# Optimization experiments

Measured on AMD Instinct MI355X. Metric: run time of the kernel, lower is better.

Reference implementation:

```python
import jax, jax.numpy as jnp
import numpy as np

B, G, N, P, E, F, K = 8, 256, 1024, 4, 1, 256, 4
ZERO_TOL = 1e-9
INF = 1e12
ATT_SLOPE = 0.2  # leaky relu slope inside attention


def setup_inputs() -> dict:
    key = jax.random.key(0)
    ks = jax.random.split(key, 6)
    stdv = float(1.0 / np.sqrt(G * P))
    x = jax.random.normal(ks[0], (B, G, N), jnp.float32)
    mixer = jax.random.uniform(ks[1], (P, E, 2 * F), jnp.float32, -stdv, stdv)
    weight = jax.random.uniform(ks[2], (P, E, F, G), jnp.float32, -stdv, stdv)
    weight_bias = jnp.zeros((P, E, F), jnp.float32)  # reset_parameters inits to 0
    filterWeight = jax.random.uniform(ks[3], (P, F, E, K, G), jnp.float32, -stdv, stdv)
    bias = jax.random.uniform(ks[4], (F, 1), jnp.float32, -stdv, stdv)
    adj = (jax.random.uniform(ks[5], (B, E, N, N)) < 0.05).astype(jnp.float32)
    S = jnp.maximum(adj, jnp.eye(N, dtype=jnp.float32)[None, None])
    return dict(x=x, mixer=mixer, weight=weight, weight_bias=weight_bias,
                filterWeight=filterWeight, bias=bias, S=S)


def reference(x, mixer, weight, weight_bias, filterWeight, bias, S):
    # --- learnAttentionGSOBatch ---
    # Wx: [B,P,E,F,N]
    Wx = jnp.einsum('pefg,bgn->bpefn', weight, x) + weight_bias[None, :, :, :, None]
    a1 = mixer[..., :F]   # [P,E,F]
    a2 = mixer[..., F:]   # [P,E,F]
    e1 = jnp.einsum('pef,bpefn->bpen', a1, Wx)  # a1^T W x_j
    e2 = jnp.einsum('pef,bpefn->bpen', a2, Wx)  # a2^T W x_i
    # aWx[b,p,e,i,j] = e1[j] + e2[i]  (matches a1Wx + a2Wx^T broadcast)
    aWx = e1[..., None, :] + e2[..., :, None]   # [B,P,E,N,N]
    eij = jax.nn.leaky_relu(aWx, ATT_SLOPE)
    mask = (jnp.sum(jnp.abs(S), axis=1)[:, None, None] > ZERO_TOL).astype(x.dtype)  # [B,1,1,N,N]
    aij = jax.nn.softmax(eij * mask - (1.0 - mask) * INF, axis=-1) * mask  # [B,P,E,N,N]

    # --- K-hop polynomial filter ---
    xk = jnp.broadcast_to(x[:, None, None], (B, P, E, G, N))
    zs = [xk]
    for _ in range(1, K):
        xk = jnp.matmul(xk, aij)        # diffuse along attention GSO
        zs.append(xk)
    z = jnp.stack(zs, axis=3)            # [B,P,E,K,G,N]
    # h reshape [P,F,E*K*G] contracted against z reshaped [B,P,N,E*K*G]
    y = jnp.einsum('bpekgn,pfekg->bpfn', z, filterWeight) + bias  # bias [F,1] broadcasts

    # --- forward wrapper: nonlinearity (leaky_relu, default slope 0.01) + head concat ---
    y = jax.nn.leaky_relu(y)                              # [B,P,F,N]
    y = jnp.transpose(y, (0, 3, 1, 2)).reshape(B, N, P * F)
    return jnp.transpose(y, (0, 2, 1))                    # [B, P*F, N]
```

## Files before the change

kernel.cpp:

```cpp
#include <hip/hip_runtime.h>
#include <hip/hip_bf16.h>

#define B_ 8
#define G_ 256
#define N_ 1024
#define P_ 4
#define F_ 256
#define KHOP 4
#define KG_ (KHOP * G_)

typedef unsigned short ushort_t;
typedef __bf16 bf16x8 __attribute__((ext_vector_type(8)));
typedef unsigned short u16x8 __attribute__((ext_vector_type(8)));
typedef float f32x4 __attribute__((ext_vector_type(4)));

__device__ __forceinline__ unsigned short f2bf(float f) {
  union { float fl; unsigned int i; } v; v.fl = f;
  return (unsigned short)((v.i + 0x7fffu + ((v.i >> 16) & 1u)) >> 16);
}

__device__ __forceinline__ void gload_lds16(const ushort_t* g, ushort_t* l) {
  __builtin_amdgcn_global_load_lds(
      (const __attribute__((address_space(1))) void*)g,
      (__attribute__((address_space(3))) void*)l, 16, 0, 0);
}

__global__ __launch_bounds__(256) void k_prep(
    const float* __restrict__ x, const float* __restrict__ mixer,
    const float* __restrict__ weight, const float* __restrict__ wb,
    const float* __restrict__ fw, float* __restrict__ e1, float* __restrict__ e2,
    ushort_t* __restrict__ fwbf, ushort_t* __restrict__ xT,
    float* __restrict__ sumb) {
  int blk = blockIdx.x;
  int t = threadIdx.x;
  if (blk < 128) {
    __shared__ float s1[G_], s2[G_];
    __shared__ float cred[2][4];
    int bp = blk >> 2;
    int nc = blk & 3;
    int b = bp >> 2, p = bp & (P_ - 1);
    int n = nc * 256 + t;
    float acc1 = 0.f, acc2 = 0.f;
    const float* wp = weight + (size_t)p * F_ * G_ + t;
    const float* mp = mixer + p * 2 * F_;
    for (int f = 0; f < F_; ++f) {
      float wv = wp[(size_t)f * G_];
      acc1 = fmaf(mp[f], wv, acc1);
      acc2 = fmaf(mp[F_ + f], wv, acc2);
    }
    s1[t] = acc1;
    s2[t] = acc2;
    float c1p = mp[t] * wb[p * F_ + t];
    float c2p = mp[F_ + t] * wb[p * F_ + t];
#pragma unroll
    for (int mask = 1; mask < 64; mask <<= 1) {
      c1p += __shfl_xor(c1p, mask, 64);
      c2p += __shfl_xor(c2p, mask, 64);
    }
    if ((t & 63) == 0) {
      cred[0][t >> 6] = c1p;
      cred[1][t >> 6] = c2p;
    }
    __syncthreads();
    float c1 = cred[0][0] + cred[0][1] + cred[0][2] + cred[0][3];
    float c2 = cred[1][0] + cred[1][1] + cred[1][2] + cred[1][3];
    const float* xb = x + (size_t)b * G_ * N_ + n;
    float a1 = 0.f, a2 = 0.f;
#pragma unroll 8
    for (int g = 0; g < G_; ++g) {
      float xv = xb[(size_t)g * N_];
      a1 = fmaf(s1[g], xv, a1);
      a2 = fmaf(s2[g], xv, a2);
    }
    e1[(size_t)bp * N_ + n] = c1 + a1;
    e2[(size_t)bp * N_ + n] = c2 + a2;
  } else if (blk < 128 + 1024) {
    int i = (blk - 128) * 1024 + t * 4;
    float4 v = *(const float4*)&fw[i];
    ushort4 o;
    o.x = f2bf(v.x); o.y = f2bf(v.y); o.z = f2bf(v.z); o.w = f2bf(v.w);
    *(ushort4*)&fwbf[i] = o;
  } else if (blk < 1152 + 512) {
    __shared__ ushort_t tile[64][66];
    int idx = blk - 1152;
    int n0 = (idx & 15) * 64;
    int g0 = ((idx >> 4) & 3) * 64;
    int b = idx >> 6;
    int rr = t >> 4, cc = (t & 15) * 4;
#pragma unroll
    for (int ps = 0; ps < 4; ++ps) {
      float4 v = *(const float4*)&x[((size_t)b * G_ + g0 + ps * 16 + rr) * N_ + n0 + cc];
      tile[ps * 16 + rr][cc] = f2bf(v.x);
      tile[ps * 16 + rr][cc + 1] = f2bf(v.y);
      tile[ps * 16 + rr][cc + 2] = f2bf(v.z);
      tile[ps * 16 + rr][cc + 3] = f2bf(v.w);
    }
    __syncthreads();
#pragma unroll
    for (int ps = 0; ps < 4; ++ps) {
      int nl = ps * 16 + rr;
      int gl = cc;
      ushort4 o;
      o.x = tile[gl][nl];
      o.y = tile[gl + 1][nl];
      o.z = tile[gl + 2][nl];
      o.w = tile[gl + 3][nl];
      *(ushort4*)&xT[((size_t)b * N_ + n0 + nl) * G_ + g0 + gl] = o;
    }
  } else {
    int i = (blk - 1664) * 256 + t;
    sumb[i] = 0.f;
  }
}

__global__ __launch_bounds__(256) void k_att(const float* __restrict__ e1,
                                             const float* __restrict__ e2,
                                             const float* __restrict__ S,
                                             ushort_t* __restrict__ expT,
                                             float* __restrict__ sumb) {
  __shared__ ushort_t tile[256][72];
  __shared__ float se1[256];
  __shared__ float se2[64];
  int bp = blockIdx.z;
  int b = bp >> 2;
  int i0 = blockIdx.y * 64;
  int jt = blockIdx.x;
  int j0 = jt * 256;
  int t = threadIdx.x;
  int rr = t >> 4;
  int cc4 = t & 15;
  int cc = cc4 * 4;

  se1[t] = e1[(size_t)bp * N_ + j0 + t];
  if (t < 64) se2[t] = e2[(size_t)bp * N_ + i0 + t];
  __syncthreads();

  const float* Sb = S + (size_t)b * N_ * N_;
  float re2[4];
#pragma unroll
  for (int ps = 0; ps < 4; ++ps) re2[ps] = se2[ps * 16 + rr];
  float psum[4] = {0.f, 0.f, 0.f, 0.f};
#pragma unroll
  for (int js = 0; js < 4; ++js) {
    float4 e1q = *(float4*)&se1[js * 64 + cc];
    float e1v[4] = {e1q.x, e1q.y, e1q.z, e1q.w};
#pragma unroll
    for (int ps = 0; ps < 4; ++ps) {
      int il = ps * 16 + rr;
      float4 s4 = *(const float4*)&Sb[(size_t)(i0 + il) * N_ + j0 + js * 64 + cc];
      float sv[4] = {s4.x, s4.y, s4.z, s4.w};
#pragma unroll
      for (int s = 0; s < 4; ++s) {
        float v = e1v[s] + re2[ps];
        float l = v >= 0.f ? v : 0.2f * v;
        bool m = fabsf(sv[s]) > 1e-9f;
        float e = m ? __expf(l) : 0.f;
        psum[ps] += e;
        tile[js * 64 + cc + s][il] = f2bf(e);
      }
    }
  }
#pragma unroll
  for (int mask = 1; mask < 16; mask <<= 1) {
#pragma unroll
    for (int ps = 0; ps < 4; ++ps) psum[ps] += __shfl_xor(psum[ps], mask, 64);
  }
  if (cc4 == 0) {
#pragma unroll
    for (int ps = 0; ps < 4; ++ps)
      atomicAdd(&sumb[(size_t)bp * N_ + i0 + ps * 16 + rr], psum[ps]);
  }
  __syncthreads();
  ushort_t* Tb = expT + (size_t)bp * N_ * N_;
  int jl0 = t >> 3;
  int ig = (t & 7) * 8;
#pragma unroll
  for (int pass = 0; pass < 8; ++pass) {
    int jl = pass * 32 + jl0;
    u16x8 v = *(const u16x8*)&tile[jl][ig];
    *(u16x8*)&Tb[(size_t)(j0 + jl) * N_ + i0 + ig] = v;
  }
}

__global__ __launch_bounds__(256, 2) void gemm_step(
    const ushort_t* __restrict__ Aprev, const ushort_t* __restrict__ Bt,
    const ushort_t* __restrict__ fwbf, const ushort_t* __restrict__ xT,
    const float* __restrict__ bias, const float* __restrict__ sumb,
    ushort_t* __restrict__ outb, float* __restrict__ outf,
    int kslice, int has_prev, int last) {
  __shared__ ushort_t As[2][128 * 32];
  __shared__ ushort_t Bs[2][128 * 32];
  int bp = blockIdx.z;
  int p = bp & (P_ - 1), b = bp >> 2;
  int n0 = blockIdx.x * 128, m0 = blockIdx.y * 128;
  int t = threadIdx.x;
  int lane = t & 63;
  int w = t >> 6;
  int wm = w >> 1, wn = w & 1;
  int lr = lane & 15, quad = lane >> 4;
  int rowL = t >> 2;
  int colL = (t & 3) * 8;
  int ldsoff = (t & ~63) * 8;

  const ushort_t* A1 = Aprev + (size_t)bp * (F_ * N_) + (size_t)(m0 + rowL) * N_ + colL;
  const ushort_t* B1 = Bt + (size_t)bp * N_ * N_ + (size_t)(n0 + rowL) * N_ + colL;
  const ushort_t* A2 = fwbf + (size_t)p * (F_ * KG_) + (size_t)(m0 + rowL) * KG_ +
                       kslice * G_ + colL;
  const ushort_t* B2 = xT + (size_t)b * (N_ * G_) + (size_t)(n0 + rowL) * G_ + colL;

  f32x4 acc[4][4] = {};

  if (has_prev) {
    for (int kt = 0; kt < N_; kt += 64) {
      __syncthreads();
      gload_lds16(A1 + kt, &As[0][ldsoff]);
      gload_lds16(A1 + (size_t)64 * N_ + kt, &As[0][2048 + ldsoff]);
      gload_lds16(A1 + kt + 32, &As[1][ldsoff]);
      gload_lds16(A1 + (size_t)64 * N_ + kt + 32, &As[1][2048 + ldsoff]);
      gload_lds16(B1 + kt, &Bs[0][ldsoff]);
      gload_lds16(B1 + (size_t)64 * N_ + kt, &Bs[0][2048 + ldsoff]);
      gload_lds16(B1 + kt + 32, &Bs[1][ldsoff]);
      gload_lds16(B1 + (size_t)64 * N_ + kt + 32, &Bs[1][2048 + ldsoff]);
      __syncthreads();
#pragma unroll
      for (int c = 0; c < 2; ++c) {
        bf16x8 af[4], bfr[4];
#pragma unroll
        for (int mi = 0; mi < 4; ++mi)
          af[mi] = __builtin_bit_cast(bf16x8,
              *(const u16x8*)&As[c][(wm * 64 + mi * 16 + lr) * 32 + quad * 8]);
#pragma unroll
        for (int ni = 0; ni < 4; ++ni)
          bfr[ni] = __builtin_bit_cast(bf16x8,
              *(const u16x8*)&Bs[c][(wn * 64 + ni * 16 + lr) * 32 + quad * 8]);
#pragma unroll
        for (int mi = 0; mi < 4; ++mi)
#pragma unroll
          for (int ni = 0; ni < 4; ++ni)
            acc[mi][ni] = __builtin_amdgcn_mfma_f32_16x16x32_bf16(af[mi], bfr[ni], acc[mi][ni], 0, 0, 0);
      }
    }
  }
  for (int gt = 0; gt < G_; gt += 64) {
    __syncthreads();
    gload_lds16(A2 + gt, &As[0][ldsoff]);
    gload_lds16(A2 + (size_t)64 * KG_ + gt, &As[0][2048 + ldsoff]);
    gload_lds16(A2 + gt + 32, &As[1][ldsoff]);
    gload_lds16(A2 + (size_t)64 * KG_ + gt + 32, &As[1][2048 + ldsoff]);
    gload_lds16(B2 + gt, &Bs[0][ldsoff]);
    gload_lds16(B2 + (size_t)64 * G_ + gt, &Bs[0][2048 + ldsoff]);
    gload_lds16(B2 + gt + 32, &Bs[1][ldsoff]);
    gload_lds16(B2 + (size_t)64 * G_ + gt + 32, &Bs[1][2048 + ldsoff]);
    __syncthreads();
#pragma unroll
    for (int c = 0; c < 2; ++c) {
      bf16x8 af[4], bfr[4];
#pragma unroll
      for (int mi = 0; mi < 4; ++mi)
        af[mi] = __builtin_bit_cast(bf16x8,
            *(const u16x8*)&As[c][(wm * 64 + mi * 16 + lr) * 32 + quad * 8]);
#pragma unroll
      for (int ni = 0; ni < 4; ++ni)
        bfr[ni] = __builtin_bit_cast(bf16x8,
            *(const u16x8*)&Bs[c][(wn * 64 + ni * 16 + lr) * 32 + quad * 8]);
#pragma unroll
      for (int mi = 0; mi < 4; ++mi)
#pragma unroll
        for (int ni = 0; ni < 4; ++ni)
          acc[mi][ni] = __builtin_amdgcn_mfma_f32_16x16x32_bf16(af[mi], bfr[ni], acc[mi][ni], 0, 0, 0);
    }
  }

  if (last) {
    float* Ob = outf + (size_t)bp * (F_ * N_);
#pragma unroll
    for (int mi = 0; mi < 4; ++mi) {
      int fbase = m0 + wm * 64 + mi * 16 + quad * 4;
#pragma unroll
      for (int ni = 0; ni < 4; ++ni) {
        int n = n0 + wn * 64 + ni * 16 + lr;
#pragma unroll
        for (int r = 0; r < 4; ++r) {
          float v = acc[mi][ni][r] + bias[fbase + r];
          Ob[(size_t)(fbase + r) * N_ + n] = v >= 0.f ? v : 0.01f * v;
        }
      }
    }
  } else {
    ushort_t* Ob = outb + (size_t)bp * (F_ * N_);
    float iv[4];
#pragma unroll
    for (int ni = 0; ni < 4; ++ni)
      iv[ni] = 1.0f / sumb[(size_t)bp * N_ + n0 + wn * 64 + ni * 16 + lr];
#pragma unroll
    for (int mi = 0; mi < 4; ++mi) {
      int fbase = m0 + wm * 64 + mi * 16 + quad * 4;
#pragma unroll
      for (int ni = 0; ni < 4; ++ni) {
        int n = n0 + wn * 64 + ni * 16 + lr;
#pragma unroll
        for (int r = 0; r < 4; ++r)
          Ob[(size_t)(fbase + r) * N_ + n] = f2bf(acc[mi][ni][r] * iv[ni]);
      }
    }
  }
}

extern "C" void kernel_launch(void* const* d_in, const int* in_sizes, int n_in,
                              void* d_out, int out_size, void* d_ws, size_t ws_size,
                              hipStream_t stream) {
  const float* x = (const float*)d_in[0];
  const float* mixer = (const float*)d_in[1];
  const float* weight = (const float*)d_in[2];
  const float* wb = (const float*)d_in[3];
  const float* fw = (const float*)d_in[4];
  const float* bias = (const float*)d_in[5];
  const float* S = (const float*)d_in[6];
  float* out = (float*)d_out;

  char* ws = (char*)d_ws;
  size_t off = 0;
  auto take = [&](size_t bytes) -> char* {
    char* p = ws + off;
    off = (off + bytes + 255) & ~(size_t)255;
    return p;
  };
  float* e1 = (float*)take((size_t)B_ * P_ * N_ * 4);
  float* e2 = (float*)take((size_t)B_ * P_ * N_ * 4);
  float* sumb = (float*)take((size_t)B_ * P_ * N_ * 4);
  ushort_t* fwbf = (ushort_t*)take((size_t)P_ * F_ * KHOP * G_ * 2);
  ushort_t* xT = (ushort_t*)take((size_t)B_ * N_ * G_ * 2);
  ushort_t* expT = (ushort_t*)take((size_t)B_ * P_ * N_ * N_ * 2);
  ushort_t* sA = (ushort_t*)take((size_t)B_ * P_ * F_ * N_ * 2);
  ushort_t* sB = (ushort_t*)take((size_t)B_ * P_ * F_ * N_ * 2);

  k_prep<<<1792, 256, 0, stream>>>(x, mixer, weight, wb, fw, e1, e2, fwbf, xT, sumb);
  k_att<<<dim3(4, 16, 32), 256, 0, stream>>>(e1, e2, S, expT, sumb);

  dim3 gg(8, 2, 32);
  gemm_step<<<gg, 256, 0, stream>>>(nullptr, expT, fwbf, xT, bias, sumb, sA, nullptr, 3, 0, 0);
  gemm_step<<<gg, 256, 0, stream>>>(sA, expT, fwbf, xT, bias, sumb, sB, nullptr, 2, 1, 0);
  gemm_step<<<gg, 256, 0, stream>>>(sB, expT, fwbf, xT, bias, sumb, sA, nullptr, 1, 1, 0);
  gemm_step<<<gg, 256, 0, stream>>>(sA, expT, fwbf, xT, bias, sumb, nullptr, out, 0, 1, 1);
}
```

Measured before the change: 258.0 us.

## Double-buffer GEMM LDS tiles and remap blocks so each XCD owns whole batches

The two K-loops of the Horner-style GEMM step are merged into one loop. Global-to-LDS loads now use a double-buffered pipeline: the next tile is issued before computing the current one, with explicit vmcnt waits and barriers. Launch is flattened to a 1D grid that maps blocks so each XCD handles four (b,p) slices, keeping each expT matrix's reuse within one L2. This doubles LDS use to 64KB per block, which may reduce occupancy under launch_bounds(256,2).

```diff
diff --git a/kernel.cpp b/kernel.cpp
--- a/kernel.cpp
+++ b/kernel.cpp
@@ -188,11 +188,16 @@
     const float* __restrict__ bias, const float* __restrict__ sumb,
     ushort_t* __restrict__ outb, float* __restrict__ outf,
     int kslice, int has_prev, int last) {
-  __shared__ ushort_t As[2][128 * 32];
-  __shared__ ushort_t Bs[2][128 * 32];
-  int bp = blockIdx.z;
+  __shared__ ushort_t As[2][2][128 * 32];
+  __shared__ ushort_t Bs[2][2][128 * 32];
+  int id = blockIdx.x;
+  int xcd = id & 7;
+  int slot = id >> 3;
+  int bp = xcd * 4 + (slot >> 4);
+  int inner = slot & 15;
+  int m0 = (inner >> 3) * 128;
+  int n0 = (inner & 7) * 128;
   int p = bp & (P_ - 1), b = bp >> 2;
-  int n0 = blockIdx.x * 128, m0 = blockIdx.y * 128;
   int t = threadIdx.x;
   int lane = t & 63;
   int w = t >> 6;
@@ -202,73 +207,69 @@
   int colL = (t & 3) * 8;
   int ldsoff = (t & ~63) * 8;
 
-  const ushort_t* A1 = Aprev + (size_t)bp * (F_ * N_) + (size_t)(m0 + rowL) * N_ + colL;
+  const ushort_t* A1 = has_prev
+      ? Aprev + (size_t)bp * (F_ * N_) + (size_t)(m0 + rowL) * N_ + colL
+      : (const ushort_t*)nullptr;
   const ushort_t* B1 = Bt + (size_t)bp * N_ * N_ + (size_t)(n0 + rowL) * N_ + colL;
   const ushort_t* A2 = fwbf + (size_t)p * (F_ * KG_) + (size_t)(m0 + rowL) * KG_ +
                        kslice * G_ + colL;
   const ushort_t* B2 = xT + (size_t)b * (N_ * G_) + (size_t)(n0 + rowL) * G_ + colL;
 
+  const int ntA = has_prev ? (N_ / 64) : 0;
+  const int NT = ntA + G_ / 64;
+
   f32x4 acc[4][4] = {};
 
-  if (has_prev) {
-    for (int kt = 0; kt < N_; kt += 64) {
-      __syncthreads();
-      gload_lds16(A1 + kt, &As[0][ldsoff]);
-      gload_lds16(A1 + (size_t)64 * N_ + kt, &As[0][2048 + ldsoff]);
-      gload_lds16(A1 + kt + 32, &As[1][ldsoff]);
-      gload_lds16(A1 + (size_t)64 * N_ + kt + 32, &As[1][2048 + ldsoff]);
-      gload_lds16(B1 + kt, &Bs[0][ldsoff]);
-      gload_lds16(B1 + (size_t)64 * N_ + kt, &Bs[0][2048 + ldsoff]);
-      gload_lds16(B1 + kt + 32, &Bs[1][ldsoff]);
-      gload_lds16(B1 + (size_t)64 * N_ + kt + 32, &Bs[1][2048 + ldsoff]);
-      __syncthreads();
-#pragma unroll
-      for (int c = 0; c < 2; ++c) {
-        bf16x8 af[4], bfr[4];
-#pragma unroll
-        for (int mi = 0; mi < 4; ++mi)
-          af[mi] = __builtin_bit_cast(bf16x8,
-              *(const u16x8*)&As[c][(wm * 64 + mi * 16 + lr) * 32 + quad * 8]);
-#pragma unroll
-        for (int ni = 0; ni < 4; ++ni)
-          bfr[ni] = __builtin_bit_cast(bf16x8,
-              *(const u16x8*)&Bs[c][(wn * 64 + ni * 16 + lr) * 32 + quad * 8]);
-#pragma unroll
-        for (int mi = 0; mi < 4; ++mi)
-#pragma unroll
-          for (int ni = 0; ni < 4; ++ni)
-            acc[mi][ni] = __builtin_amdgcn_mfma_f32_16x16x32_bf16(af[mi], bfr[ni], acc[mi][ni], 0, 0, 0);
-      }
-    }
-  }
-  for (int gt = 0; gt < G_; gt += 64) {
-    __syncthreads();
-    gload_lds16(A2 + gt, &As[0][ldsoff]);
-    gload_lds16(A2 + (size_t)64 * KG_ + gt, &As[0][2048 + ldsoff]);
-    gload_lds16(A2 + gt + 32, &As[1][ldsoff]);
-    gload_lds16(A2 + (size_t)64 * KG_ + gt + 32, &As[1][2048 + ldsoff]);
-    gload_lds16(B2 + gt, &Bs[0][ldsoff]);
-    gload_lds16(B2 + (size_t)64 * G_ + gt, &Bs[0][2048 + ldsoff]);
-    gload_lds16(B2 + gt + 32, &Bs[1][ldsoff]);
-    gload_lds16(B2 + (size_t)64 * G_ + gt + 32, &Bs[1][2048 + ldsoff]);
-    __syncthreads();
+  auto stage = [&](int buf, int it) {
+    const ushort_t *Ab, *Bb;
+    size_t ldA, ldB;
+    int ko;
+    if (it < ntA) {
+      Ab = A1; ldA = N_; Bb = B1; ldB = N_; ko = it * 64;
+    } else {
+      Ab = A2; ldA = KG_; Bb = B2; ldB = G_; ko = (it - ntA) * 64;
+    }
+    gload_lds16(Ab + ko,                 &As[buf][0][ldsoff]);
+    gload_lds16(Ab + 64 * ldA + ko,      &As[buf][0][2048 + ldsoff]);
+    gload_lds16(Ab + ko + 32,            &As[buf][1][ldsoff]);
+    gload_lds16(Ab + 64 * ldA + ko + 32, &As[buf][1][2048 + ldsoff]);
+    gload_lds16(Bb + ko,                 &Bs[buf][0][ldsoff]);
+    gload_lds16(Bb + 64 * ldB + ko,      &Bs[buf][0][2048 + ldsoff]);
+    gload_lds16(Bb + ko + 32,            &Bs[buf][1][ldsoff]);
+    gload_lds16(Bb + 64 * ldB + ko + 32, &Bs[buf][1][2048 + ldsoff]);
+  };
+
+  stage(0, 0);
+  int buf = 0;
+  for (int it = 0; it < NT; ++it) {
+    if (it + 1 < NT) {
+      stage(buf ^ 1, it + 1);
+      asm volatile("s_waitcnt vmcnt(8)" ::: "memory");
+    } else {
+      asm volatile("s_waitcnt vmcnt(0)" ::: "memory");
+    }
+    __builtin_amdgcn_s_barrier();
+    asm volatile("" ::: "memory");
 #pragma unroll
     for (int c = 0; c < 2; ++c) {
       bf16x8 af[4], bfr[4];
 #pragma unroll
       for (int mi = 0; mi < 4; ++mi)
         af[mi] = __builtin_bit_cast(bf16x8,
-            *(const u16x8*)&As[c][(wm * 64 + mi * 16 + lr) * 32 + quad * 8]);
+            *(const u16x8*)&As[buf][c][(wm * 64 + mi * 16 + lr) * 32 + quad * 8]);
 #pragma unroll
       for (int ni = 0; ni < 4; ++ni)
         bfr[ni] = __builtin_bit_cast(bf16x8,
-            *(const u16x8*)&Bs[c][(wn * 64 + ni * 16 + lr) * 32 + quad * 8]);
+            *(const u16x8*)&Bs[buf][c][(wn * 64 + ni * 16 + lr) * 32 + quad * 8]);
 #pragma unroll
       for (int mi = 0; mi < 4; ++mi)
 #pragma unroll
         for (int ni = 0; ni < 4; ++ni)
           acc[mi][ni] = __builtin_amdgcn_mfma_f32_16x16x32_bf16(af[mi], bfr[ni], acc[mi][ni], 0, 0, 0);
     }
+    asm volatile("" ::: "memory");
+    __builtin_amdgcn_s_barrier();
+    buf ^= 1;
   }
 
   if (last) {
@@ -337,9 +338,8 @@
   k_prep<<<1792, 256, 0, stream>>>(x, mixer, weight, wb, fw, e1, e2, fwbf, xT, sumb);
   k_att<<<dim3(4, 16, 32), 256, 0, stream>>>(e1, e2, S, expT, sumb);
 
-  dim3 gg(8, 2, 32);
-  gemm_step<<<gg, 256, 0, stream>>>(nullptr, expT, fwbf, xT, bias, sumb, sA, nullptr, 3, 0, 0);
-  gemm_step<<<gg, 256, 0, stream>>>(sA, expT, fwbf, xT, bias, sumb, sB, nullptr, 2, 1, 0);
-  gemm_step<<<gg, 256, 0, stream>>>(sB, expT, fwbf, xT, bias, sumb, sA, nullptr, 1, 1, 0);
-  gemm_step<<<gg, 256, 0, stream>>>(sA, expT, fwbf, xT, bias, sumb, nullptr, out, 0, 1, 1);
-}
+  gemm_step<<<512, 256, 0, stream>>>(nullptr, expT, fwbf, xT, bias, sumb, sA, nullptr, 3, 0, 0);
+  gemm_step<<<512, 256, 0, stream>>>(sA, expT, fwbf, xT, bias, sumb, sB, nullptr, 2, 1, 0);
+  gemm_step<<<512, 256, 0, stream>>>(sB, expT, fwbf, xT, bias, sumb, sA, nullptr, 1, 1, 0);
+  gemm_step<<<512, 256, 0, stream>>>(sA, expT, fwbf, xT, bias, sumb, nullptr, out, 0, 1, 1);
+}
```

After: 232.4 us. 1.11x faster.
